# Optimization experiments

Measured on AMD Instinct MI355X. Metric: run time of the kernel, lower is better.

The kernel has to match this reference:

```python
import jax, jax.numpy as jnp
import numpy as np

QMAX = 7.0   # int4 symmetric, narrow range [-7, 7] per weight; acts use [-8, 7]
QMIN = -8.0

def _ste_quant(v, scale, qmin, qmax):
    """Symmetric per-tensor fake-quant with straight-through estimator."""
    s = jax.lax.stop_gradient(scale)
    q = jnp.clip(jnp.round(v / s), qmin, qmax) * s
    return v + jax.lax.stop_gradient(q - v)


def setup_inputs() -> dict:
    key = jax.random.key(0)
    k1, k2, k3 = jax.random.split(key, 3)
    d_model, vocab = 1024, 50257
    x = jax.random.normal(k1, (2, 1024, d_model), jnp.float32)
    W = jax.random.normal(k2, (vocab, d_model), jnp.float32) * 0.02
    b = jax.random.normal(k3, (vocab,), jnp.float32) * 0.01
    return {"x": x, "W": W, "b": b}


def reference(x, W, b):
    # Activation quant: 4-bit signed, per-tensor scale from max-abs stats
    sx = jnp.max(jnp.abs(x)) / QMAX
    xq = _ste_quant(x, sx, QMIN, QMAX)
    # Weight quant: 4-bit signed per-tensor
    sw = jnp.max(jnp.abs(W)) / QMAX
    wq = _ste_quant(W, sw, QMIN, QMAX)
    # Int32 bias: quantized at the accumulator scale sx*sw (range huge -> round only)
    sb = jax.lax.stop_gradient(sx * sw)
    bq = b + jax.lax.stop_gradient(jnp.round(b / sb) * sb - b)
    # Quantized GEMM with int32-style accumulation, expressed as dequantized matmul
    logits = jnp.einsum('bsd,vd->bsv', xq, wq) + bq  # [B, S, vocab]
    return jax.nn.log_softmax(logits, axis=-1)
```

## Files before the change

### kernel.cpp

```cpp
#include <hip/hip_runtime.h>
#include <hip/hip_bf16.h>

#define N_VOCAB 50257
#define NB      393
#define N_PAD   50304
#define D_K     1024
#define M_ROWS  2048
#define GEMM_BLOCKS (NB * 16)
#define PER_XCD     (GEMM_BLOCKS/8)

typedef __attribute__((ext_vector_type(4))) int i32x4;

__device__ inline void async_copy16(const void* g, void* l) {
  auto* gp = (const __attribute__((address_space(1))) unsigned int*)g;
  auto* lp = (__attribute__((address_space(3))) unsigned int*)l;
  __builtin_amdgcn_global_load_lds(gp, lp, 16, 0, 0);
}

__device__ inline signed char qint(float v, float s) {
  float q = fminf(fmaxf(rintf(v / s), -8.f), 7.f);
  return (signed char)(int)q;
}

__global__ void absmax2_kernel(const float4* __restrict__ x, int nx4,
                               const float4* __restrict__ Wp, int nw4,
                               unsigned* __restrict__ amax) {
  const bool isx = blockIdx.x < 512;
  const float4* p = isx ? x : Wp;
  const int n4 = isx ? nx4 : nw4;
  const int b0 = isx ? blockIdx.x : blockIdx.x - 512;
  const int nb = isx ? 512 : (gridDim.x - 512);
  float m = 0.f;
  for (int i = b0 * blockDim.x + threadIdx.x; i < n4; i += nb * blockDim.x) {
    float4 v = p[i];
    m = fmaxf(m, fmaxf(fmaxf(fabsf(v.x), fabsf(v.y)),
                       fmaxf(fabsf(v.z), fabsf(v.w))));
  }
#pragma unroll
  for (int off = 32; off; off >>= 1) m = fmaxf(m, __shfl_xor(m, off));
  __shared__ float red[4];
  int tid = threadIdx.x;
  if ((tid & 63) == 0) red[tid >> 6] = m;
  __syncthreads();
  if (tid == 0) {
    m = fmaxf(fmaxf(red[0], red[1]), fmaxf(red[2], red[3]));
    atomicMax(&amax[isx ? 0 : 1], __float_as_uint(m));
  }
}

__global__ void quant_kernel(const float4* __restrict__ x,
                             const float4* __restrict__ Wp,
                             const float* __restrict__ b,
                             char4* __restrict__ qx, char4* __restrict__ qw,
                             float* __restrict__ bq,
                             const unsigned* __restrict__ amax) {
  const int bid = blockIdx.x;
  const int tid = threadIdx.x;
  const int nw4 = (N_VOCAB * D_K) / 4;
  if (bid < 2048) {
    int i = bid * 256 + tid;
    float s = __uint_as_float(amax[0]) * (1.0f / 7.0f);
    float4 v = x[i];
    char4 q;
    q.x = qint(v.x, s); q.y = qint(v.y, s);
    q.z = qint(v.z, s); q.w = qint(v.w, s);
    qx[i] = q;
  } else if (bid < 2048 + 50304) {
    int i = (bid - 2048) * 256 + tid;
    char4 q = {0, 0, 0, 0};
    if (i < nw4) {
      float s = __uint_as_float(amax[1]) * (1.0f / 7.0f);
      float4 v = Wp[i];
      q.x = qint(v.x, s); q.y = qint(v.y, s);
      q.z = qint(v.z, s); q.w = qint(v.w, s);
    }
    qw[i] = q;
  } else {
    int i = (bid - (2048 + 50304)) * 256 + tid;
    if (i < N_PAD) {
      float v = 0.f;
      if (i < N_VOCAB) {
        float sb = (__uint_as_float(amax[0]) * (1.0f / 7.0f)) *
                   (__uint_as_float(amax[1]) * (1.0f / 7.0f));
        v = rintf(b[i] / sb) * sb;
      }
      bq[i] = v;
    }
  }
}

__global__ __launch_bounds__(256, 4) void gemm_kernel(
    const signed char* __restrict__ qx,
    const signed char* __restrict__ qw,
    const float* __restrict__ bq,
    const unsigned* __restrict__ amax,
    float* __restrict__ outp,
    float* __restrict__ pmax,
    float* __restrict__ psum)
{
  constexpr int BK = 64;
  constexpr int NT = D_K / BK;
  __shared__ __align__(16) signed char sA[2][128 * BK];
  __shared__ __align__(16) signed char sB[3][128 * BK];

  const int tid = threadIdx.x;
  const int l = tid & 63;
  const int w = tid >> 6;
  const int wr = w >> 1, wc = w & 1;

  const int bid = blockIdx.x;
  const int vb = (bid & 7) * PER_XCD + (bid >> 3);
  const int nb = vb >> 4;
  const int m0 = (vb & 15) * 128;
  const int n0 = nb * 128;

  const float sx = __uint_as_float(amax[0]) * (1.0f / 7.0f);
  const float sw = __uint_as_float(amax[1]) * (1.0f / 7.0f);
  const float scale = sx * sw;

  i32x4 acc[4][4] = {};

  const int srow = l >> 2;
  const int scol = ((l & 3) ^ ((l >> 3) & 3)) * 16;

  auto stageA = [&](int buf, int kt) {
    int k0 = kt * BK;
#pragma unroll
    for (int i = 0; i < 2; ++i) {
      int c = w * 2 + i;
      int row = c * 16 + srow;
      async_copy16(qx + (size_t)(m0 + row) * D_K + k0 + scol,
                   &sA[buf][c * 1024]);
    }
  };
  auto stageB = [&](int buf, int kt) {
    int k0 = kt * BK;
#pragma unroll
    for (int i = 0; i < 2; ++i) {
      int c = w * 2 + i;
      int row = c * 16 + srow;
      async_copy16(qw + (size_t)(n0 + row) * D_K + k0 + scol,
                   &sB[buf][c * 1024]);
    }
  };

  stageA(0, 0);
  stageB(0, 0);
  stageB(1, 1);
  asm volatile("s_waitcnt vmcnt(2)" ::: "memory");
  __builtin_amdgcn_s_barrier();
  __builtin_amdgcn_sched_barrier(0);

#pragma unroll
  for (int kt = 0; kt < NT; ++kt) {
    const int ca = kt & 1;
    const int cb = kt % 3;

    i32x4 af[4], bfr[4];
#pragma unroll
    for (int mi = 0; mi < 4; ++mi) {
      int row = wr * 64 + mi * 16 + (l & 15);
      int kb = ((l >> 4) ^ ((row >> 1) & 3)) * 16;
      af[mi] = *(const i32x4*)&sA[ca][row * BK + kb];
    }
#pragma unroll
    for (int ni = 0; ni < 4; ++ni) {
      int row = wc * 64 + ni * 16 + (l & 15);
      int kb = ((l >> 4) ^ ((row >> 1) & 3)) * 16;
      bfr[ni] = *(const i32x4*)&sB[cb][row * BK + kb];
    }

    if (kt + 1 < NT) stageA(ca ^ 1, kt + 1);
    if (kt + 2 < NT) stageB((kt + 2) % 3, kt + 2);

    __builtin_amdgcn_s_setprio(1);
#pragma unroll
    for (int mi = 0; mi < 4; ++mi)
#pragma unroll
      for (int ni = 0; ni < 4; ++ni)
        acc[mi][ni] = __builtin_amdgcn_mfma_i32_16x16x64_i8(
            af[mi], bfr[ni], acc[mi][ni], 0, 0, 0);
    __builtin_amdgcn_s_setprio(0);
    __builtin_amdgcn_sched_barrier(0);

    if (kt + 1 < NT) {
      if (kt + 2 < NT)
        asm volatile("s_waitcnt vmcnt(2)" ::: "memory");
      else
        asm volatile("s_waitcnt vmcnt(0)" ::: "memory");
      __builtin_amdgcn_s_barrier();
      __builtin_amdgcn_sched_barrier(0);
    }
  }

  bool valid[4];
  float bb[4];
#pragma unroll
  for (int ni = 0; ni < 4; ++ni) {
    int col = n0 + wc * 64 + ni * 16 + (l & 15);
    valid[ni] = (col < N_VOCAB);
    bb[ni] = valid[ni] ? bq[col] : 0.f;
  }
  float lg[4][4][4];
#pragma unroll
  for (int mi = 0; mi < 4; ++mi)
#pragma unroll
    for (int ni = 0; ni < 4; ++ni)
#pragma unroll
      for (int r = 0; r < 4; ++r)
        lg[mi][ni][r] = (float)acc[mi][ni][r] * scale + bb[ni];

  __syncthreads();
  float* redMax = (float*)&sB[0][0];
  float* redSum = redMax + 256;

  float rmax[4][4];
#pragma unroll
  for (int mi = 0; mi < 4; ++mi)
#pragma unroll
    for (int r = 0; r < 4; ++r) {
      float mval = -3.4e38f;
#pragma unroll
      for (int ni = 0; ni < 4; ++ni)
        if (valid[ni]) mval = fmaxf(mval, lg[mi][ni][r]);
#pragma unroll
      for (int off = 1; off < 16; off <<= 1)
        mval = fmaxf(mval, __shfl_xor(mval, off));
      rmax[mi][r] = mval;
      if ((l & 15) == 0)
        redMax[(wr * 64 + mi * 16 + (l >> 4) * 4 + r) * 2 + wc] = mval;
    }
  __syncthreads();

#pragma unroll
  for (int mi = 0; mi < 4; ++mi)
#pragma unroll
    for (int r = 0; r < 4; ++r) {
      int rl = wr * 64 + mi * 16 + (l >> 4) * 4 + r;
      float gmax = fmaxf(redMax[rl * 2 + 0], redMax[rl * 2 + 1]);
      float s = 0.f;
#pragma unroll
      for (int ni = 0; ni < 4; ++ni)
        if (valid[ni]) s += __expf(lg[mi][ni][r] - gmax);
#pragma unroll
      for (int off = 1; off < 16; off <<= 1)
        s += __shfl_xor(s, off);
      if ((l & 15) == 0) redSum[rl * 2 + wc] = s;
      rmax[mi][r] = gmax;
    }
  __syncthreads();

  if (wc == 0 && (l & 15) == 0) {
#pragma unroll
    for (int mi = 0; mi < 4; ++mi)
#pragma unroll
      for (int r = 0; r < 4; ++r) {
        int rl = wr * 64 + mi * 16 + (l >> 4) * 4 + r;
        int rowg = m0 + rl;
        pmax[(size_t)rowg * NB + nb] = rmax[mi][r];
        psum[(size_t)rowg * NB + nb] = redSum[rl * 2 + 0] + redSum[rl * 2 + 1];
      }
  }

#pragma unroll
  for (int mi = 0; mi < 4; ++mi)
#pragma unroll
    for (int r = 0; r < 4; ++r) {
      int rowg = m0 + wr * 64 + mi * 16 + (l >> 4) * 4 + r;
      size_t rb = (size_t)rowg * N_VOCAB;
#pragma unroll
      for (int ni = 0; ni < 4; ++ni) {
        if (valid[ni]) {
          int col = n0 + wc * 64 + ni * 16 + (l & 15);
          outp[rb + col] = lg[mi][ni][r];
        }
      }
    }
}

__global__ __launch_bounds__(256) void logz_sub_kernel(
    const float* __restrict__ pmax, const float* __restrict__ psum,
    float* __restrict__ out) {
  const int row = blockIdx.x;
  const float* pm = pmax + (size_t)row * NB;
  const float* ps = psum + (size_t)row * NB;
  const int tid = threadIdx.x;
  __shared__ float red[9];

  float m = -3.4e38f;
  for (int i = tid; i < NB; i += 256) m = fmaxf(m, pm[i]);
#pragma unroll
  for (int off = 32; off; off >>= 1) m = fmaxf(m, __shfl_xor(m, off));
  if ((tid & 63) == 0) red[tid >> 6] = m;
  __syncthreads();
  m = fmaxf(fmaxf(red[0], red[1]), fmaxf(red[2], red[3]));

  float s = 0.f;
  for (int i = tid; i < NB; i += 256) s += ps[i] * __expf(pm[i] - m);
#pragma unroll
  for (int off = 32; off; off >>= 1) s += __shfl_xor(s, off);
  if ((tid & 63) == 0) red[4 + (tid >> 6)] = s;
  __syncthreads();
  if (tid == 0) {
    s = red[4] + red[5] + red[6] + red[7];
    red[8] = m + __logf(s);
  }
  __syncthreads();
  const float lz = red[8];

  const size_t base = (size_t)row * N_VOCAB;
  const int a = (4 - (row & 3)) & 3;
  if (tid < a) out[base + tid] -= lz;
  const int n4 = (N_VOCAB - a) >> 2;
  float4* p = (float4*)(out + base + a);
  for (int i = tid; i < n4; i += 256) {
    float4 v = p[i];
    v.x -= lz; v.y -= lz; v.z -= lz; v.w -= lz;
    p[i] = v;
  }
  const int done = a + n4 * 4;
  if (tid < N_VOCAB - done) out[base + done + tid] -= lz;
}

extern "C" void kernel_launch(void* const* d_in, const int* in_sizes, int n_in,
                              void* d_out, int out_size, void* d_ws,
                              size_t ws_size, hipStream_t stream) {
  const float* x = (const float*)d_in[0];
  const float* W = (const float*)d_in[1];
  const float* b = (const float*)d_in[2];
  float* out = (float*)d_out;

  char* ws = (char*)d_ws;
  unsigned* amax = (unsigned*)ws;
  float* bq = (float*)(ws + 4096);
  float* pmax = (float*)(ws + (2ull << 20));
  float* psum = (float*)(ws + (6ull << 20));
  signed char* qx = (signed char*)(ws + (10ull << 20));
  signed char* qw = (signed char*)(ws + (14ull << 20));

  hipMemsetAsync(amax, 0, 8, stream);

  const int nx4 = (M_ROWS * D_K) / 4;
  const int nw4 = (N_VOCAB * D_K) / 4;

  absmax2_kernel<<<2560, 256, 0, stream>>>((const float4*)x, nx4,
                                           (const float4*)W, nw4, amax);

  quant_kernel<<<2048 + 50304 + 197, 256, 0, stream>>>(
      (const float4*)x, (const float4*)W, b, (char4*)qx, (char4*)qw, bq, amax);

  gemm_kernel<<<GEMM_BLOCKS, 256, 0, stream>>>(qx, qw, bq, amax, out, pmax,
                                               psum);

  logz_sub_kernel<<<M_ROWS, 256, 0, stream>>>(pmax, psum, out);
}
```

Before: 553.3 us.

## Triple-buffer A tiles and interleave LDS loads, prefetch, and MFMA in quarters

Moves the A tile to a 3-stage LDS ring like B and prefetches both two k-steps ahead. Splits each k-step into four 2x2 MFMA sub-blocks, each with its own LDS reads, one async global copy and barriers, in a ping-pong style schedule. The aim is to overlap LDS reads and global loads with MFMA work more finely. In exchange it uses more LDS, drops occupancy to 3 blocks, and adds many extra barriers per k-step.

```diff
diff --git a/kernel.cpp b/kernel.cpp
--- a/kernel.cpp
+++ b/kernel.cpp
@@ -89,7 +89,7 @@
   }
 }
 
-__global__ __launch_bounds__(256, 4) void gemm_kernel(
+__global__ __launch_bounds__(256, 3) void gemm_kernel(
     const signed char* __restrict__ qx,
     const signed char* __restrict__ qw,
     const float* __restrict__ bq,
@@ -100,7 +100,7 @@
 {
   constexpr int BK = 64;
   constexpr int NT = D_K / BK;
-  __shared__ __align__(16) signed char sA[2][128 * BK];
+  __shared__ __align__(16) signed char sA[3][128 * BK];
   __shared__ __align__(16) signed char sB[3][128 * BK];
 
   const int tid = threadIdx.x;
@@ -123,73 +123,88 @@
   const int srow = l >> 2;
   const int scol = ((l & 3) ^ ((l >> 3) & 3)) * 16;
 
-  auto stageA = [&](int buf, int kt) {
-    int k0 = kt * BK;
-#pragma unroll
-    for (int i = 0; i < 2; ++i) {
-      int c = w * 2 + i;
-      int row = c * 16 + srow;
-      async_copy16(qx + (size_t)(m0 + row) * D_K + k0 + scol,
-                   &sA[buf][c * 1024]);
-    }
+  auto stA = [&](int buf, int kt, int i) {
+    int c = w * 2 + i;
+    int row = c * 16 + srow;
+    async_copy16(qx + (size_t)(m0 + row) * D_K + kt * BK + scol,
+                 &sA[buf][c * 1024]);
   };
-  auto stageB = [&](int buf, int kt) {
-    int k0 = kt * BK;
-#pragma unroll
-    for (int i = 0; i < 2; ++i) {
-      int c = w * 2 + i;
-      int row = c * 16 + srow;
-      async_copy16(qw + (size_t)(n0 + row) * D_K + k0 + scol,
-                   &sB[buf][c * 1024]);
-    }
+  auto stB = [&](int buf, int kt, int i) {
+    int c = w * 2 + i;
+    int row = c * 16 + srow;
+    async_copy16(qw + (size_t)(n0 + row) * D_K + kt * BK + scol,
+                 &sB[buf][c * 1024]);
   };
 
-  stageA(0, 0);
-  stageB(0, 0);
-  stageB(1, 1);
-  asm volatile("s_waitcnt vmcnt(2)" ::: "memory");
+  stA(0, 0, 0); stA(0, 0, 1); stB(0, 0, 0); stB(0, 0, 1);
+  stA(1, 1, 0); stA(1, 1, 1); stB(1, 1, 0); stB(1, 1, 1);
+  asm volatile("s_waitcnt vmcnt(4)" ::: "memory");
   __builtin_amdgcn_s_barrier();
   __builtin_amdgcn_sched_barrier(0);
 
 #pragma unroll
   for (int kt = 0; kt < NT; ++kt) {
-    const int ca = kt & 1;
-    const int cb = kt % 3;
-
-    i32x4 af[4], bfr[4];
-#pragma unroll
-    for (int mi = 0; mi < 4; ++mi) {
-      int row = wr * 64 + mi * 16 + (l & 15);
-      int kb = ((l >> 4) ^ ((row >> 1) & 3)) * 16;
-      af[mi] = *(const i32x4*)&sA[ca][row * BK + kb];
-    }
-#pragma unroll
-    for (int ni = 0; ni < 4; ++ni) {
-      int row = wc * 64 + ni * 16 + (l & 15);
-      int kb = ((l >> 4) ^ ((row >> 1) & 3)) * 16;
-      bfr[ni] = *(const i32x4*)&sB[cb][row * BK + kb];
-    }
-
-    if (kt + 1 < NT) stageA(ca ^ 1, kt + 1);
-    if (kt + 2 < NT) stageB((kt + 2) % 3, kt + 2);
-
-    __builtin_amdgcn_s_setprio(1);
-#pragma unroll
-    for (int mi = 0; mi < 4; ++mi)
-#pragma unroll
-      for (int ni = 0; ni < 4; ++ni)
-        acc[mi][ni] = __builtin_amdgcn_mfma_i32_16x16x64_i8(
-            af[mi], bfr[ni], acc[mi][ni], 0, 0, 0);
-    __builtin_amdgcn_s_setprio(0);
-    __builtin_amdgcn_sched_barrier(0);
-
-    if (kt + 1 < NT) {
-      if (kt + 2 < NT)
-        asm volatile("s_waitcnt vmcnt(2)" ::: "memory");
-      else
-        asm volatile("s_waitcnt vmcnt(0)" ::: "memory");
+    const int cur = kt % 3;
+    const int nx2 = (kt + 2) % 3;
+    const bool pf = (kt + 2 < NT);
+
+#pragma unroll
+    for (int q = 0; q < 4; ++q) {
+      const int mi2 = (q >> 1) * 2;
+      const int ni2 = (q & 1) * 2;
+
+      i32x4 a0, a1, b0, b1;
+      {
+        int row0 = wr * 64 + (mi2 + 0) * 16 + (l & 15);
+        int row1 = wr * 64 + (mi2 + 1) * 16 + (l & 15);
+        int k0 = ((l >> 4) ^ ((row0 >> 1) & 3)) * 16;
+        int k1 = ((l >> 4) ^ ((row1 >> 1) & 3)) * 16;
+        a0 = *(const i32x4*)&sA[cur][row0 * BK + k0];
+        a1 = *(const i32x4*)&sA[cur][row1 * BK + k1];
+      }
+      {
+        int row0 = wc * 64 + (ni2 + 0) * 16 + (l & 15);
+        int row1 = wc * 64 + (ni2 + 1) * 16 + (l & 15);
+        int k0 = ((l >> 4) ^ ((row0 >> 1) & 3)) * 16;
+        int k1 = ((l >> 4) ^ ((row1 >> 1) & 3)) * 16;
+        b0 = *(const i32x4*)&sB[cur][row0 * BK + k0];
+        b1 = *(const i32x4*)&sB[cur][row1 * BK + k1];
+      }
+
+      if (pf) {
+        if (q == 0) stA(nx2, kt + 2, 0);
+        if (q == 1) stA(nx2, kt + 2, 1);
+        if (q == 2) stB(nx2, kt + 2, 0);
+        if (q == 3) stB(nx2, kt + 2, 1);
+      }
+
       __builtin_amdgcn_s_barrier();
+      asm volatile("s_waitcnt lgkmcnt(0)" ::: "memory");
       __builtin_amdgcn_sched_barrier(0);
+      __builtin_amdgcn_s_setprio(1);
+      acc[mi2 + 0][ni2 + 0] = __builtin_amdgcn_mfma_i32_16x16x64_i8(
+          a0, b0, acc[mi2 + 0][ni2 + 0], 0, 0, 0);
+      acc[mi2 + 0][ni2 + 1] = __builtin_amdgcn_mfma_i32_16x16x64_i8(
+          a0, b1, acc[mi2 + 0][ni2 + 1], 0, 0, 0);
+      acc[mi2 + 1][ni2 + 0] = __builtin_amdgcn_mfma_i32_16x16x64_i8(
+          a1, b0, acc[mi2 + 1][ni2 + 0], 0, 0, 0);
+      acc[mi2 + 1][ni2 + 1] = __builtin_amdgcn_mfma_i32_16x16x64_i8(
+          a1, b1, acc[mi2 + 1][ni2 + 1], 0, 0, 0);
+      __builtin_amdgcn_s_setprio(0);
+
+      if (q == 3) {
+        if (kt + 1 < NT) {
+          if (pf)
+            asm volatile("s_waitcnt vmcnt(4)" ::: "memory");
+          else
+            asm volatile("s_waitcnt vmcnt(0)" ::: "memory");
+          __builtin_amdgcn_s_barrier();
+          __builtin_amdgcn_sched_barrier(0);
+        }
+      } else {
+        __builtin_amdgcn_s_barrier();
+        __builtin_amdgcn_sched_barrier(0);
+      }
     }
   }
 
```

Result: slower. 625.8 us (+13.1%).

## Enlarge GEMM tile to 256x256 with 8 waves and split-phase pipelining

Applied to the files above, without the earlier changes.

The int8 GEMM moves from 128x128 tiles with 4 waves to 256x256 tiles with 8 waves (512 threads). Each K step is split into two half-phases, with A and B prefetch interleaved between MFMA groups and barriers, over triple-buffered LDS. Larger tiles raise arithmetic intensity per loaded byte and halve the number of partial softmax columns, but use much more LDS (96KB) and registers. Occupancy drops to about one block per CU, and the extra barriers per iteration may cost latency.

```diff
diff --git a/kernel.cpp b/kernel.cpp
--- a/kernel.cpp
+++ b/kernel.cpp
@@ -2,12 +2,11 @@
 #include <hip/hip_bf16.h>
 
 #define N_VOCAB 50257
-#define NB      393
-#define N_PAD   50304
+#define NBC     197
+#define N_PAD   50432
 #define D_K     1024
 #define M_ROWS  2048
-#define GEMM_BLOCKS (NB * 16)
-#define PER_XCD     (GEMM_BLOCKS/8)
+#define GEMM_BLOCKS (NBC * 8)
 
 typedef __attribute__((ext_vector_type(4))) int i32x4;
 
@@ -65,7 +64,7 @@
     q.x = qint(v.x, s); q.y = qint(v.y, s);
     q.z = qint(v.z, s); q.w = qint(v.w, s);
     qx[i] = q;
-  } else if (bid < 2048 + 50304) {
+  } else if (bid < 2048 + 50432) {
     int i = (bid - 2048) * 256 + tid;
     char4 q = {0, 0, 0, 0};
     if (i < nw4) {
@@ -76,7 +75,7 @@
     }
     qw[i] = q;
   } else {
-    int i = (bid - (2048 + 50304)) * 256 + tid;
+    int i = (bid - (2048 + 50432)) * 256 + tid;
     if (i < N_PAD) {
       float v = 0.f;
       if (i < N_VOCAB) {
@@ -89,7 +88,7 @@
   }
 }
 
-__global__ __launch_bounds__(256, 4) void gemm_kernel(
+__global__ __launch_bounds__(512, 2) void gemm_kernel(
     const signed char* __restrict__ qx,
     const signed char* __restrict__ qw,
     const float* __restrict__ bq,
@@ -100,79 +99,69 @@
 {
   constexpr int BK = 64;
   constexpr int NT = D_K / BK;
-  __shared__ __align__(16) signed char sA[2][128 * BK];
-  __shared__ __align__(16) signed char sB[3][128 * BK];
+  __shared__ __align__(16) signed char sA[3][256 * BK];
+  __shared__ __align__(16) signed char sB[3][256 * BK];
 
   const int tid = threadIdx.x;
   const int l = tid & 63;
   const int w = tid >> 6;
-  const int wr = w >> 1, wc = w & 1;
+  const int wr = w >> 2;
+  const int wc = w & 3;
 
   const int bid = blockIdx.x;
-  const int vb = (bid & 7) * PER_XCD + (bid >> 3);
-  const int nb = vb >> 4;
-  const int m0 = (vb & 15) * 128;
-  const int n0 = nb * 128;
+  const int vb = (bid & 7) * NBC + (bid >> 3);
+  const int nb = vb >> 3;
+  const int m0 = (vb & 7) * 256;
+  const int n0 = nb * 256;
 
   const float sx = __uint_as_float(amax[0]) * (1.0f / 7.0f);
   const float sw = __uint_as_float(amax[1]) * (1.0f / 7.0f);
   const float scale = sx * sw;
 
-  i32x4 acc[4][4] = {};
-
-  const int srow = l >> 2;
+  i32x4 acc[8][4] = {};
+
   const int scol = ((l & 3) ^ ((l >> 3) & 3)) * 16;
 
-  auto stageA = [&](int buf, int kt) {
-    int k0 = kt * BK;
-#pragma unroll
-    for (int i = 0; i < 2; ++i) {
-      int c = w * 2 + i;
-      int row = c * 16 + srow;
-      async_copy16(qx + (size_t)(m0 + row) * D_K + k0 + scol,
-                   &sA[buf][c * 1024]);
-    }
+  auto stA = [&](int buf, int kt, int h) {
+    int row = h * 128 + w * 16 + (l >> 2);
+    async_copy16(qx + (size_t)(m0 + row) * D_K + kt * BK + scol,
+                 &sA[buf][(h * 128 + w * 16) * BK]);
   };
-  auto stageB = [&](int buf, int kt) {
-    int k0 = kt * BK;
-#pragma unroll
-    for (int i = 0; i < 2; ++i) {
-      int c = w * 2 + i;
-      int row = c * 16 + srow;
-      async_copy16(qw + (size_t)(n0 + row) * D_K + k0 + scol,
-                   &sB[buf][c * 1024]);
-    }
+  auto stB = [&](int buf, int kt, int h) {
+    int row = h * 128 + w * 16 + (l >> 2);
+    async_copy16(qw + (size_t)(n0 + row) * D_K + kt * BK + scol,
+                 &sB[buf][(h * 128 + w * 16) * BK]);
   };
 
-  stageA(0, 0);
-  stageB(0, 0);
-  stageB(1, 1);
-  asm volatile("s_waitcnt vmcnt(2)" ::: "memory");
+  stA(0, 0, 0); stA(0, 0, 1); stB(0, 0, 0); stB(0, 0, 1);
+  stA(1, 1, 0); stA(1, 1, 1); stB(1, 1, 0); stB(1, 1, 1);
+  asm volatile("s_waitcnt vmcnt(4)" ::: "memory");
   __builtin_amdgcn_s_barrier();
   __builtin_amdgcn_sched_barrier(0);
 
-#pragma unroll
+  int cur = 0;
   for (int kt = 0; kt < NT; ++kt) {
-    const int ca = kt & 1;
-    const int cb = kt % 3;
-
-    i32x4 af[4], bfr[4];
-#pragma unroll
-    for (int mi = 0; mi < 4; ++mi) {
-      int row = wr * 64 + mi * 16 + (l & 15);
-      int kb = ((l >> 4) ^ ((row >> 1) & 3)) * 16;
-      af[mi] = *(const i32x4*)&sA[ca][row * BK + kb];
-    }
+    int nxt = cur + 2; if (nxt >= 3) nxt -= 3;
+    const bool pf = (kt + 2 < NT);
+
+    i32x4 bfr[4], af[4];
 #pragma unroll
     for (int ni = 0; ni < 4; ++ni) {
       int row = wc * 64 + ni * 16 + (l & 15);
       int kb = ((l >> 4) ^ ((row >> 1) & 3)) * 16;
-      bfr[ni] = *(const i32x4*)&sB[cb][row * BK + kb];
-    }
-
-    if (kt + 1 < NT) stageA(ca ^ 1, kt + 1);
-    if (kt + 2 < NT) stageB((kt + 2) % 3, kt + 2);
-
+      bfr[ni] = *(const i32x4*)&sB[cur][row * BK + kb];
+    }
+#pragma unroll
+    for (int mi = 0; mi < 4; ++mi) {
+      int row = wr * 128 + mi * 16 + (l & 15);
+      int kb = ((l >> 4) ^ ((row >> 1) & 3)) * 16;
+      af[mi] = *(const i32x4*)&sA[cur][row * BK + kb];
+    }
+    if (pf) { stA(nxt, kt + 2, 0); stA(nxt, kt + 2, 1); }
+
+    __builtin_amdgcn_s_barrier();
+    asm volatile("s_waitcnt lgkmcnt(0)" ::: "memory");
+    __builtin_amdgcn_sched_barrier(0);
     __builtin_amdgcn_s_setprio(1);
 #pragma unroll
     for (int mi = 0; mi < 4; ++mi)
@@ -182,113 +171,133 @@
             af[mi], bfr[ni], acc[mi][ni], 0, 0, 0);
     __builtin_amdgcn_s_setprio(0);
     __builtin_amdgcn_sched_barrier(0);
+    __builtin_amdgcn_s_barrier();
+    __builtin_amdgcn_sched_barrier(0);
+
+#pragma unroll
+    for (int mi = 0; mi < 4; ++mi) {
+      int row = wr * 128 + (mi + 4) * 16 + (l & 15);
+      int kb = ((l >> 4) ^ ((row >> 1) & 3)) * 16;
+      af[mi] = *(const i32x4*)&sA[cur][row * BK + kb];
+    }
+    if (pf) { stB(nxt, kt + 2, 0); stB(nxt, kt + 2, 1); }
+
+    __builtin_amdgcn_s_barrier();
+    asm volatile("s_waitcnt lgkmcnt(0)" ::: "memory");
+    __builtin_amdgcn_sched_barrier(0);
+    __builtin_amdgcn_s_setprio(1);
+#pragma unroll
+    for (int mi = 0; mi < 4; ++mi)
+#pragma unroll
+      for (int ni = 0; ni < 4; ++ni)
+        acc[mi + 4][ni] = __builtin_amdgcn_mfma_i32_16x16x64_i8(
+            af[mi], bfr[ni], acc[mi + 4][ni], 0, 0, 0);
+    __builtin_amdgcn_s_setprio(0);
+    __builtin_amdgcn_sched_barrier(0);
 
     if (kt + 1 < NT) {
-      if (kt + 2 < NT)
-        asm volatile("s_waitcnt vmcnt(2)" ::: "memory");
+      if (pf)
+        asm volatile("s_waitcnt vmcnt(4)" ::: "memory");
       else
         asm volatile("s_waitcnt vmcnt(0)" ::: "memory");
       __builtin_amdgcn_s_barrier();
       __builtin_amdgcn_sched_barrier(0);
     }
+    cur += 1; if (cur == 3) cur = 0;
   }
 
   bool valid[4];
-  float bb[4];
+  float bb4[4];
 #pragma unroll
   for (int ni = 0; ni < 4; ++ni) {
     int col = n0 + wc * 64 + ni * 16 + (l & 15);
     valid[ni] = (col < N_VOCAB);
-    bb[ni] = valid[ni] ? bq[col] : 0.f;
-  }
-  float lg[4][4][4];
-#pragma unroll
-  for (int mi = 0; mi < 4; ++mi)
-#pragma unroll
-    for (int ni = 0; ni < 4; ++ni)
-#pragma unroll
-      for (int r = 0; r < 4; ++r)
-        lg[mi][ni][r] = (float)acc[mi][ni][r] * scale + bb[ni];
-
-  __syncthreads();
-  float* redMax = (float*)&sB[0][0];
-  float* redSum = redMax + 256;
-
-  float rmax[4][4];
-#pragma unroll
-  for (int mi = 0; mi < 4; ++mi)
+    bb4[ni] = valid[ni] ? bq[col] : 0.f;
+  }
+#define LGT(mi, ni, r) ((float)acc[mi][ni][r] * scale + bb4[ni])
+
+  __syncthreads();
+  float* redMax = (float*)&sA[0][0];
+  float* redSum = redMax + 1024;
+
+  float gm[8][4];
+#pragma unroll
+  for (int mi = 0; mi < 8; ++mi)
 #pragma unroll
     for (int r = 0; r < 4; ++r) {
       float mval = -3.4e38f;
 #pragma unroll
       for (int ni = 0; ni < 4; ++ni)
-        if (valid[ni]) mval = fmaxf(mval, lg[mi][ni][r]);
+        if (valid[ni]) mval = fmaxf(mval, LGT(mi, ni, r));
 #pragma unroll
       for (int off = 1; off < 16; off <<= 1)
         mval = fmaxf(mval, __shfl_xor(mval, off));
-      rmax[mi][r] = mval;
       if ((l & 15) == 0)
-        redMax[(wr * 64 + mi * 16 + (l >> 4) * 4 + r) * 2 + wc] = mval;
-    }
-  __syncthreads();
-
-#pragma unroll
-  for (int mi = 0; mi < 4; ++mi)
+        redMax[(wr * 128 + mi * 16 + (l >> 4) * 4 + r) * 4 + wc] = mval;
+    }
+  __syncthreads();
+
+#pragma unroll
+  for (int mi = 0; mi < 8; ++mi)
 #pragma unroll
     for (int r = 0; r < 4; ++r) {
-      int rl = wr * 64 + mi * 16 + (l >> 4) * 4 + r;
-      float gmax = fmaxf(redMax[rl * 2 + 0], redMax[rl * 2 + 1]);
+      int rl = wr * 128 + mi * 16 + (l >> 4) * 4 + r;
+      float gmax = fmaxf(fmaxf(redMax[rl * 4 + 0], redMax[rl * 4 + 1]),
+                         fmaxf(redMax[rl * 4 + 2], redMax[rl * 4 + 3]));
       float s = 0.f;
 #pragma unroll
       for (int ni = 0; ni < 4; ++ni)
-        if (valid[ni]) s += __expf(lg[mi][ni][r] - gmax);
+        if (valid[ni]) s += __expf(LGT(mi, ni, r) - gmax);
 #pragma unroll
       for (int off = 1; off < 16; off <<= 1)
         s += __shfl_xor(s, off);
-      if ((l & 15) == 0) redSum[rl * 2 + wc] = s;
-      rmax[mi][r] = gmax;
+      if ((l & 15) == 0) redSum[rl * 4 + wc] = s;
+      gm[mi][r] = gmax;
     }
   __syncthreads();
 
   if (wc == 0 && (l & 15) == 0) {
 #pragma unroll
-    for (int mi = 0; mi < 4; ++mi)
+    for (int mi = 0; mi < 8; ++mi)
 #pragma unroll
       for (int r = 0; r < 4; ++r) {
-        int rl = wr * 64 + mi * 16 + (l >> 4) * 4 + r;
+        int rl = wr * 128 + mi * 16 + (l >> 4) * 4 + r;
         int rowg = m0 + rl;
-        pmax[(size_t)rowg * NB + nb] = rmax[mi][r];
-        psum[(size_t)rowg * NB + nb] = redSum[rl * 2 + 0] + redSum[rl * 2 + 1];
+        pmax[(size_t)rowg * NBC + nb] = gm[mi][r];
+        psum[(size_t)rowg * NBC + nb] =
+            (redSum[rl * 4 + 0] + redSum[rl * 4 + 1]) +
+            (redSum[rl * 4 + 2] + redSum[rl * 4 + 3]);
       }
   }
 
 #pragma unroll
-  for (int mi = 0; mi < 4; ++mi)
+  for (int mi = 0; mi < 8; ++mi)
 #pragma unroll
     for (int r = 0; r < 4; ++r) {
-      int rowg = m0 + wr * 64 + mi * 16 + (l >> 4) * 4 + r;
+      int rowg = m0 + wr * 128 + mi * 16 + (l >> 4) * 4 + r;
       size_t rb = (size_t)rowg * N_VOCAB;
 #pragma unroll
       for (int ni = 0; ni < 4; ++ni) {
         if (valid[ni]) {
           int col = n0 + wc * 64 + ni * 16 + (l & 15);
-          outp[rb + col] = lg[mi][ni][r];
+          outp[rb + col] = LGT(mi, ni, r);
         }
       }
     }
+#undef LGT
 }
 
 __global__ __launch_bounds__(256) void logz_sub_kernel(
     const float* __restrict__ pmax, const float* __restrict__ psum,
     float* __restrict__ out) {
   const int row = blockIdx.x;
-  const float* pm = pmax + (size_t)row * NB;
-  const float* ps = psum + (size_t)row * NB;
+  const float* pm = pmax + (size_t)row * NBC;
+  const float* ps = psum + (size_t)row * NBC;
   const int tid = threadIdx.x;
   __shared__ float red[9];
 
   float m = -3.4e38f;
-  for (int i = tid; i < NB; i += 256) m = fmaxf(m, pm[i]);
+  for (int i = tid; i < NBC; i += 256) m = fmaxf(m, pm[i]);
 #pragma unroll
   for (int off = 32; off; off >>= 1) m = fmaxf(m, __shfl_xor(m, off));
   if ((tid & 63) == 0) red[tid >> 6] = m;
@@ -296,7 +305,7 @@
   m = fmaxf(fmaxf(red[0], red[1]), fmaxf(red[2], red[3]));
 
   float s = 0.f;
-  for (int i = tid; i < NB; i += 256) s += ps[i] * __expf(pm[i] - m);
+  for (int i = tid; i < NBC; i += 256) s += ps[i] * __expf(pm[i] - m);
 #pragma unroll
   for (int off = 32; off; off >>= 1) s += __shfl_xor(s, off);
   if ((tid & 63) == 0) red[4 + (tid >> 6)] = s;
@@ -346,10 +355,10 @@
   absmax2_kernel<<<2560, 256, 0, stream>>>((const float4*)x, nx4,
                                            (const float4*)W, nw4, amax);
 
-  quant_kernel<<<2048 + 50304 + 197, 256, 0, stream>>>(
+  quant_kernel<<<2048 + 50432 + 197, 256, 0, stream>>>(
       (const float4*)x, (const float4*)W, b, (char4*)qx, (char4*)qw, bq, amax);
 
-  gemm_kernel<<<GEMM_BLOCKS, 256, 0, stream>>>(qx, qw, bq, amax, out, pmax,
+  gemm_kernel<<<GEMM_BLOCKS, 512, 0, stream>>>(qx, qw, bq, amax, out, pmax,
                                                psum);
 
   logz_sub_kernel<<<M_ROWS, 256, 0, stream>>>(pmax, psum, out);
```

Result: slower. 615.5 us (+11.2%).
